# Kernel tuning notes

Measured on AMD Instinct MI355X. Metric: run time of the kernel, lower is better.

## Reference

```python
import jax, jax.numpy as jnp
import numpy as np

D_MODEL, D_K, D_FF, N = 1024, 128, 4096, 8192

def _linear_params(key, fan_in, fan_out):
    # mimic torch nn.Linear default init (uniform +/- 1/sqrt(fan_in))
    k1, k2 = jax.random.split(key)
    bound = 1.0 / np.sqrt(fan_in)
    W = jax.random.uniform(k1, (fan_out, fan_in), jnp.float32, -bound, bound)
    b = jax.random.uniform(k2, (fan_out,), jnp.float32, -bound, bound)
    return W, b

def setup_inputs() -> dict:
    key = jax.random.key(0)
    ks = jax.random.split(key, 7)
    x = jax.random.normal(ks[0], (N, D_MODEL), jnp.float32)
    Wq, bq = _linear_params(ks[1], D_MODEL, D_K)
    Wk, bk = _linear_params(ks[2], D_MODEL, D_K)
    Wv, bv = _linear_params(ks[3], D_MODEL, D_K)
    Wp, bp = _linear_params(ks[4], D_K, D_MODEL)
    W1, b1 = _linear_params(ks[5], D_MODEL, D_FF)
    W2, b2 = _linear_params(ks[6], D_FF, D_MODEL)
    return {"x": x, "Wq": Wq, "bq": bq, "Wk": Wk, "bk": bk, "Wv": Wv, "bv": bv,
            "Wp": Wp, "bp": bp, "W1": W1, "b1": b1, "W2": W2, "b2": b2}

def reference(x, Wq, bq, Wk, bk, Wv, bv, Wp, bp, W1, b1, W2, b2):
    # projections (torch Linear: x @ W.T + b)
    Q = x @ Wq.T + bq            # [n, d_k]
    K = x @ Wk.T + bk            # [n, d_k]
    V = x @ Wv.T + bv            # [n, d_k]
    # linear attention, original evaluation order: (Q @ K^T) @ V
    attn = Q @ K.T               # [n, n]
    context = attn @ V           # [n, d_k]
    out = context @ Wp.T + bp    # [n, d_model]
    x = x + out                  # residual 1
    h = jax.nn.relu(x @ W1.T + b1)  # [n, d_ff]
    return x + (h @ W2.T + b2)   # residual 2
```

## Files before the change

kernel.cpp:

```cpp
#include <hip/hip_runtime.h>


#define MROWS 8192
#define DMODEL 1024
#define DK 128
#define DFF 4096

typedef __attribute__((ext_vector_type(8))) __bf16 bf16x8;
typedef __attribute__((ext_vector_type(4))) float f32x4;

#define BAR()     __builtin_amdgcn_s_barrier()
#define WAITV(n)  asm volatile("s_waitcnt vmcnt(" #n ")" ::: "memory")
#define LGKMC(n)  asm volatile("s_waitcnt lgkmcnt(" #n ")" ::: "memory")
#define SCHED0()  __builtin_amdgcn_sched_barrier(0)
#define GLOAD(src, dst) __builtin_amdgcn_global_load_lds( \
    (const __attribute__((address_space(1))) void*)(src), \
    (__attribute__((address_space(3))) void*)(dst), 16, 0, 0)

#define LDSO(p) ((unsigned)(unsigned long long) \
    (__attribute__((address_space(3))) const char*)(const char*)(p))

__device__ __forceinline__ bf16x8 ldsr(unsigned off) {
    bf16x8 r;
    asm volatile("ds_read_b128 %0, %1" : "=v"(r) : "v"(off));
    return r;
}

__device__ __forceinline__ void cast_one(const float* s, __bf16* d, int i) {
    const float4 a = reinterpret_cast<const float4*>(s)[2 * i];
    const float4 b = reinterpret_cast<const float4*>(s)[2 * i + 1];
    bf16x8 o;
    o[0] = (__bf16)a.x; o[1] = (__bf16)a.y; o[2] = (__bf16)a.z; o[3] = (__bf16)a.w;
    o[4] = (__bf16)b.x; o[5] = (__bf16)b.y; o[6] = (__bf16)b.z; o[7] = (__bf16)b.w;
    reinterpret_cast<bf16x8*>(d)[i] = o;
}

__global__ __launch_bounds__(256) void cast6(
    const float* __restrict__ s0, __bf16* __restrict__ d0,
    const float* __restrict__ s1, __bf16* __restrict__ d1,
    const float* __restrict__ s2, __bf16* __restrict__ d2,
    const float* __restrict__ s3, __bf16* __restrict__ d3,
    const float* __restrict__ s4, __bf16* __restrict__ d4,
    const float* __restrict__ s5, __bf16* __restrict__ d5)
{
    const int b = blockIdx.x, t = threadIdx.x;
    if      (b <  64)  cast_one(s0, d0, b * 256 + t);
    else if (b < 128)  cast_one(s1, d1, (b - 64) * 256 + t);
    else if (b < 192)  cast_one(s2, d2, (b - 128) * 256 + t);
    else if (b < 256)  cast_one(s3, d3, (b - 192) * 256 + t);
    else if (b < 2304) cast_one(s4, d4, (b - 256) * 256 + t);
    else               cast_one(s5, d5, (b - 2304) * 256 + t);
}

__global__ void pack_bias3(const float* __restrict__ a, const float* __restrict__ b,
                           const float* __restrict__ c, float* __restrict__ o)
{
    const int t = threadIdx.x;
    o[t] = a[t]; o[128 + t] = b[t]; o[256 + t] = c[t];
}

__global__ __launch_bounds__(256) void ffn2_reduce2(
    float* __restrict__ y, const __bf16* __restrict__ x2b,
    const __bf16* __restrict__ P0, const __bf16* __restrict__ P1,
    const float* __restrict__ b2, int n8)
{
    for (int i = blockIdx.x * blockDim.x + threadIdx.x; i < n8;
         i += gridDim.x * blockDim.x) {
        const int col0 = (i << 3) & (DMODEL - 1);
        const float4 ba = *reinterpret_cast<const float4*>(&b2[col0]);
        const float4 bb = *reinterpret_cast<const float4*>(&b2[col0 + 4]);
        const bf16x8 xx = reinterpret_cast<const bf16x8*>(x2b)[i];
        const bf16x8 p0 = reinterpret_cast<const bf16x8*>(P0)[i];
        const bf16x8 p1 = reinterpret_cast<const bf16x8*>(P1)[i];
        float4 o0, o1;
        o0.x = (float)xx[0] + (float)p0[0] + (float)p1[0] + ba.x;
        o0.y = (float)xx[1] + (float)p0[1] + (float)p1[1] + ba.y;
        o0.z = (float)xx[2] + (float)p0[2] + (float)p1[2] + ba.z;
        o0.w = (float)xx[3] + (float)p0[3] + (float)p1[3] + ba.w;
        o1.x = (float)xx[4] + (float)p0[4] + (float)p1[4] + bb.x;
        o1.y = (float)xx[5] + (float)p0[5] + (float)p1[5] + bb.y;
        o1.z = (float)xx[6] + (float)p0[6] + (float)p1[6] + bb.z;
        o1.w = (float)xx[7] + (float)p0[7] + (float)p1[7] + bb.w;
        reinterpret_cast<float4*>(y)[2 * i]     = o0;
        reinterpret_cast<float4*>(y)[2 * i + 1] = o1;
    }
}

template<bool RELU, bool RESID, bool BIAS, bool OUTBF, bool DUAL, bool F32A>
__global__ __launch_bounds__(256) void gemm128(
    const void* __restrict__ Ap, int lda,
    const __bf16* __restrict__ W,
    const float* __restrict__ bias,
    const float* __restrict__ resid,
    void* __restrict__ Cout, __bf16* __restrict__ Cbf, int ldc, int K)
{
    constexpr int BK = 32;
    __shared__ __bf16 As[128 * BK];
    __shared__ __bf16 Bs[128 * BK];

    const int tid  = threadIdx.x;
    const int lane = tid & 63;
    const int w    = tid >> 6;
    const int wm   = w >> 1;
    const int wn   = w & 1;
    const int fr   = lane & 15;
    const int fq   = lane >> 4;

    const long row0 = (long)blockIdx.y * 128;
    const long col0 = (long)blockIdx.x * 128;

    const int sr = (w << 4) + (lane >> 2);
    const int sc = (lane & 3) << 3;

    const __bf16* gA0 = F32A ? nullptr : (const __bf16*)Ap + (row0 + sr) * (long)lda + sc;
    const __bf16* gA1 = F32A ? nullptr : (const __bf16*)Ap + (row0 + 64 + sr) * (long)lda + sc;
    const float*  gAf = F32A ? (const float*)Ap + (row0 + (tid >> 1)) * (long)lda
                               + ((tid & 1) << 4)
                             : nullptr;
    const __bf16* gW0 = W + (col0 + sr) * (long)K + sc;
    const __bf16* gW1 = W + (col0 + 64 + sr) * (long)K + sc;

    __bf16* lA0 = &As[(w << 4) * BK];
    __bf16* lA1 = &As[((w << 4) + 64) * BK];
    __bf16* lB0 = &Bs[(w << 4) * BK];
    __bf16* lB1 = &Bs[((w << 4) + 64) * BK];

    f32x4 acc[4][4] = {};

    for (int k0 = 0; k0 < K; k0 += BK) {
        if constexpr (F32A) {
            const float* s = gAf + k0;
            const float4 f0 = reinterpret_cast<const float4*>(s)[0];
            const float4 f1 = reinterpret_cast<const float4*>(s)[1];
            const float4 f2 = reinterpret_cast<const float4*>(s)[2];
            const float4 f3 = reinterpret_cast<const float4*>(s)[3];
            bf16x8 o0, o1;
            o0[0] = (__bf16)f0.x; o0[1] = (__bf16)f0.y; o0[2] = (__bf16)f0.z; o0[3] = (__bf16)f0.w;
            o0[4] = (__bf16)f1.x; o0[5] = (__bf16)f1.y; o0[6] = (__bf16)f1.z; o0[7] = (__bf16)f1.w;
            o1[0] = (__bf16)f2.x; o1[1] = (__bf16)f2.y; o1[2] = (__bf16)f2.z; o1[3] = (__bf16)f2.w;
            o1[4] = (__bf16)f3.x; o1[5] = (__bf16)f3.y; o1[6] = (__bf16)f3.z; o1[7] = (__bf16)f3.w;
            const int ar = tid >> 1, ac = (tid & 1) << 4;
            *reinterpret_cast<bf16x8*>(&As[ar * BK + ac])     = o0;
            *reinterpret_cast<bf16x8*>(&As[ar * BK + ac + 8]) = o1;
        } else {
            GLOAD(gA0 + k0, lA0);
            GLOAD(gA1 + k0, lA1);
        }
        GLOAD(gW0 + k0, lB0);
        GLOAD(gW1 + k0, lB1);
        __syncthreads();

        bf16x8 af[4], bfr[4];
        #pragma unroll
        for (int m = 0; m < 4; m++)
            af[m] = *reinterpret_cast<const bf16x8*>(
                &As[(wm * 64 + m * 16 + fr) * BK + fq * 8]);
        #pragma unroll
        for (int n = 0; n < 4; n++)
            bfr[n] = *reinterpret_cast<const bf16x8*>(
                &Bs[(wn * 64 + n * 16 + fr) * BK + fq * 8]);

        #pragma unroll
        for (int m = 0; m < 4; m++)
            #pragma unroll
            for (int n = 0; n < 4; n++)
                acc[m][n] = __builtin_amdgcn_mfma_f32_16x16x32_bf16(
                    af[m], bfr[n], acc[m][n], 0, 0, 0);
        __syncthreads();
    }

    float bc[4];
    #pragma unroll
    for (int n = 0; n < 4; n++)
        bc[n] = BIAS ? bias[col0 + wn * 64 + n * 16 + fr] : 0.0f;
    #pragma unroll
    for (int m = 0; m < 4; m++) {
        #pragma unroll
        for (int j = 0; j < 4; j++) {
            const long r = row0 + wm * 64 + m * 16 + fq * 4 + j;
            #pragma unroll
            for (int n = 0; n < 4; n++) {
                const long c = col0 + wn * 64 + n * 16 + fr;
                float v = acc[m][n][j] + bc[n];
                if constexpr (RESID) v += resid[r * ldc + c];
                if constexpr (RELU)  v = fmaxf(v, 0.0f);
                if constexpr (OUTBF) ((__bf16*)Cout)[r * ldc + c] = (__bf16)v;
                else                 ((float*)Cout)[r * ldc + c] = v;
                if constexpr (DUAL)  Cbf[r * ldc + c] = (__bf16)v;
            }
        }
    }
}

#define RD_B()                                             \
    _Pragma("unroll")                                      \
    for (int n = 0; n < 4; n++) {                          \
        bb[n][0] = ldsr(pB + rb0 + n * 2048);              \
        bb[n][1] = ldsr(pB + rb1 + n * 2048);              \
    }
#define RD_A(m0_, cnt_)                                    \
    _Pragma("unroll")                                      \
    for (int m = m0_; m < m0_ + cnt_; m++) {               \
        a[m][0] = ldsr(pA + rb0 + m * 2048);               \
        a[m][1] = ldsr(pA + rb1 + m * 2048);               \
    }
#define MFMA2(m0_)                                                            \
    _Pragma("unroll")                                                         \
    for (int m = m0_; m < m0_ + 2; m++)                                       \
        _Pragma("unroll")                                                     \
        for (int n = 0; n < 4; n++) {                                         \
            acc[m][n] = __builtin_amdgcn_mfma_f32_16x16x32_bf16(              \
                a[m][0], bb[n][0], acc[m][n], 0, 0, 0);                       \
            acc[m][n] = __builtin_amdgcn_mfma_f32_16x16x32_bf16(              \
                a[m][1], bb[n][1], acc[m][n], 0, 0, 0);                       \
        }

template<bool RELU, bool BIAS>
__global__ __launch_bounds__(256, 2) void gemm256x128(
    const __bf16* __restrict__ A, int lda,
    const __bf16* __restrict__ W, int ldw,
    const float* __restrict__ bias,
    __bf16* __restrict__ Cout, long sstride, int ldc,
    int klen, int nb, int nbx)
{
    __shared__ char lds[49152];

    const int bid = blockIdx.x;
    const int sid = bid / nb;
    const int ib  = bid % nb;
    const int chunk = nb >> 3;
    const int swz   = (ib & 7) * chunk + (ib >> 3);
    const int bx    = swz % nbx;
    const int by    = swz / nbx;

    const long row0 = (long)by * 256;
    const long col0 = (long)bx * 128;

    const __bf16* Ash = A + (long)sid * klen;
    const __bf16* Wsh = W + (long)sid * klen;

    const int tid  = threadIdx.x;
    const int lane = tid & 63;
    const int w    = tid >> 6;
    const int wm   = w >> 1;
    const int wn   = w & 1;
    const int fr   = lane & 15;
    const int fq   = lane >> 4;

    const int scole = ((lane & 7) ^ (lane >> 3)) << 3;
    const __bf16* gA = Ash + (row0 + w * 8 + (lane >> 3)) * (long)lda + scole;
    const __bf16* gB = Wsh + (col0 + w * 8 + (lane >> 3)) * (long)ldw + scole;

    char* ldsc = &lds[0];
    const unsigned lbase = LDSO(ldsc);
    const int nt = klen >> 6;

    auto stage = [&](int t) {
        const __bf16* ap = gA + (long)t * 64;
        const __bf16* bp = gB + (long)t * 64;
        #pragma unroll
        for (int r = 0; r < 8; r++)
            GLOAD(ap + (long)(32 * r) * lda, ldsc + r * 4096 + (w << 10));
        #pragma unroll
        for (int r = 0; r < 4; r++)
            GLOAD(bp + (long)(32 * r) * ldw, ldsc + 32768 + r * 4096 + (w << 10));
    };

    const unsigned rb0 = fr * 128 + ((fq * 16) ^ ((fr & 7) << 4));
    const unsigned rb1 = fr * 128 + ((64 + fq * 16) ^ ((fr & 7) << 4));
    const unsigned pA = lbase + (wm << 14);
    const unsigned pB = lbase + 32768 + (wn << 13);

    f32x4 acc[8][4] = {};
    bf16x8 a[8][2], bb[4][2];

    for (int t = 0; t < nt; ++t) {
        stage(t);
        WAITV(0);
        BAR();

        RD_B();
        RD_A(0, 8);

        LGKMC(12); SCHED0();
        __builtin_amdgcn_s_setprio(1); MFMA2(0); __builtin_amdgcn_s_setprio(0);
        LGKMC(8); SCHED0();
        __builtin_amdgcn_s_setprio(1); MFMA2(2); __builtin_amdgcn_s_setprio(0);
        LGKMC(4); SCHED0();
        __builtin_amdgcn_s_setprio(1); MFMA2(4); __builtin_amdgcn_s_setprio(0);
        LGKMC(0); SCHED0();
        __builtin_amdgcn_s_setprio(1); MFMA2(6); __builtin_amdgcn_s_setprio(0);

        BAR();
    }

    __bf16* Cb = Cout + (long)sid * sstride;
    float bc[4];
    #pragma unroll
    for (int n = 0; n < 4; n++)
        bc[n] = BIAS ? bias[col0 + wn * 64 + n * 16 + fr] : 0.0f;

    __bf16* sw = reinterpret_cast<__bf16*>(ldsc) + (w << 12);
    const long crow0 = row0 + wm * 128;
    const long ccol0 = col0 + wn * 64;
    #pragma unroll
    for (int half = 0; half < 2; half++) {
        #pragma unroll
        for (int m = 0; m < 4; m++)
            #pragma unroll
            for (int j = 0; j < 4; j++) {
                const int row = m * 16 + fq * 4 + j;
                #pragma unroll
                for (int n = 0; n < 4; n++) {
                    float v = acc[half * 4 + m][n][j] + bc[n];
                    if constexpr (RELU) v = fmaxf(v, 0.0f);
                    sw[row * 64 + n * 16 + fr] = (__bf16)v;
                }
            }
        #pragma unroll
        for (int i = 0; i < 8; i++) {
            const bf16x8 vv = *reinterpret_cast<const bf16x8*>(sw + i * 512 + lane * 8);
            const int r  = half * 64 + i * 8 + (lane >> 3);
            const int cg = (lane & 7) << 3;
            *reinterpret_cast<bf16x8*>(&Cb[(crow0 + r) * (long)ldc + ccol0 + cg]) = vv;
        }
        __builtin_amdgcn_s_waitcnt(0);
    }
}

__global__ __launch_bounds__(256) void ktv_partial(
    const __bf16* __restrict__ Kp, const __bf16* __restrict__ Vp,
    int ld, float* __restrict__ part)
{
    __shared__ float ks[32][DK];
    __shared__ float vs[32][DK];
    const int tid = threadIdx.x;
    const int ti  = tid >> 4;
    const int tj  = tid & 15;
    float acc[8][8] = {};
    const long base = (long)blockIdx.x * 128;

    for (int n0 = 0; n0 < 128; n0 += 32) {
        for (int t = tid; t < 512; t += 256) {
            const int r  = t >> 4;
            const int cc = (t & 15) << 3;
            const bf16x8 k8 = *reinterpret_cast<const bf16x8*>(
                &Kp[(base + n0 + r) * (long)ld + cc]);
            const bf16x8 v8 = *reinterpret_cast<const bf16x8*>(
                &Vp[(base + n0 + r) * (long)ld + cc]);
            #pragma unroll
            for (int u = 0; u < 8; u++) {
                ks[r][cc + u] = (float)k8[u];
                vs[r][cc + u] = (float)v8[u];
            }
        }
        __syncthreads();
        for (int n = 0; n < 32; n++) {
            float kk[8], vv[8];
            #pragma unroll
            for (int i = 0; i < 8; i++) kk[i] = ks[n][(ti << 3) + i];
            #pragma unroll
            for (int j = 0; j < 8; j++) vv[j] = vs[n][(tj << 3) + j];
            #pragma unroll
            for (int i = 0; i < 8; i++)
                #pragma unroll
                for (int j = 0; j < 8; j++)
                    acc[i][j] = fmaf(kk[i], vv[j], acc[i][j]);
        }
        __syncthreads();
    }

    float* dst = &part[(long)blockIdx.x * (DK * DK)];
    #pragma unroll
    for (int i = 0; i < 8; i++) {
        const int ig = (ti << 3) + i;
        *reinterpret_cast<float4*>(&dst[ig * DK + (tj << 3)]) =
            make_float4(acc[i][0], acc[i][1], acc[i][2], acc[i][3]);
        *reinterpret_cast<float4*>(&dst[ig * DK + (tj << 3) + 4]) =
            make_float4(acc[i][4], acc[i][5], acc[i][6], acc[i][7]);
    }
}

__global__ __launch_bounds__(256) void ktv_reduce(
    const float* __restrict__ part, __bf16* __restrict__ ktvR)
{
    const int t = blockIdx.x * 256 + threadIdx.x;
    float s = 0.0f;
    for (int b = 0; b < 64; b++) s += part[(long)b * (DK * DK) + t];
    ktvR[t] = (__bf16)s;
}

extern "C" void kernel_launch(void* const* d_in, const int* in_sizes, int n_in,
                              void* d_out, int out_size, void* d_ws, size_t ws_size,
                              hipStream_t stream) {
    const float* x  = (const float*)d_in[0];
    const float* Wq = (const float*)d_in[1];
    const float* bq = (const float*)d_in[2];
    const float* Wk = (const float*)d_in[3];
    const float* bk = (const float*)d_in[4];
    const float* Wv = (const float*)d_in[5];
    const float* bv = (const float*)d_in[6];
    const float* Wp = (const float*)d_in[7];
    const float* bp = (const float*)d_in[8];
    const float* W1 = (const float*)d_in[9];
    const float* b1 = (const float*)d_in[10];
    const float* W2 = (const float*)d_in[11];
    const float* b2 = (const float*)d_in[12];
    float* out = (float*)d_out;

    char* ws = (char*)d_ws;
    const size_t MB = 1ull << 20;
    __bf16* P0b   = (__bf16*)(ws);
    __bf16* P1b   = P0b + (long)MROWS * DMODEL;
    __bf16* x2b   = (__bf16*)(ws +  34 * MB);
    __bf16* Hb    = (__bf16*)(ws +  51 * MB);
    __bf16* QKVb  = (__bf16*)(ws + 119 * MB);
    __bf16* W1b   = (__bf16*)(ws + 126 * MB);
    __bf16* W2b   = (__bf16*)(ws + 135 * MB);
    __bf16* Wqkvb = (__bf16*)(ws + 144 * MB);
    __bf16* Wpb   = (__bf16*)(ws + 145 * MB);
    float*  Part  = (float*) (ws + 146 * MB);
    __bf16* KtvRb = (__bf16*)(ws + 151 * MB);
    __bf16* MtB   = (__bf16*)(ws + 152 * MB);
    float*  bqkvf = (float*) (ws + 155 * MB);

    const dim3 blk(256);

    cast6<<<4352, blk, 0, stream>>>(
        Wq, Wqkvb, Wk, Wqkvb + DK * DMODEL, Wv, Wqkvb + 2 * DK * DMODEL,
        Wp, Wpb, W1, W1b, W2, W2b);
    pack_bias3<<<1, 128, 0, stream>>>(bq, bk, bv, bqkvf);

    gemm128<false,false,true,true,false,true><<<dim3(3, 64), blk, 0, stream>>>(
        x, DMODEL, Wqkvb, bqkvf, nullptr, QKVb, nullptr, 3 * DK, DMODEL);

    ktv_partial<<<64, blk, 0, stream>>>(QKVb + DK, QKVb + 2 * DK, 3 * DK, Part);
    ktv_reduce <<<64, blk, 0, stream>>>(Part, KtvRb);

    gemm128<false,false,false,true,false,false><<<dim3(1, 8), blk, 0, stream>>>(
        Wpb, DK, KtvRb, nullptr, nullptr, MtB, nullptr, DK, DK);

    gemm128<false,true,true,true,false,false><<<dim3(8, 64), blk, 0, stream>>>(
        QKVb, 3 * DK, MtB, bp, x, x2b, nullptr, DMODEL, DK);

    gemm256x128<true,true><<<1024, blk, 0, stream>>>(
        x2b, DMODEL, W1b, DMODEL, b1, Hb, 0, DFF, DMODEL, 1024, DFF / 128);

    gemm256x128<false,false><<<512, blk, 0, stream>>>(
        Hb, DFF, W2b, DFF, nullptr, P0b,
        (long)MROWS * DMODEL, DMODEL, DFF / 2, 256, DMODEL / 128);

    ffn2_reduce2<<<2048, blk, 0, stream>>>(out, x2b, P0b, P1b, b2,
                                           MROWS * DMODEL / 8);
}
```

Baseline: 223.8 us.

## Double-buffer FFN GEMM LDS with K=32 stages and prefetch next tile

The FFN GEMM kernel switches from a single-buffered K=64 tile loop to a double-buffered K=32 loop. The next stage's global-to-LDS loads are issued right after the barrier, so they overlap the current stage's MFMAs, and the trailing per-iteration barrier is removed. The staging and swizzle layout is changed to match the 32-wide rows. The cost is twice as many iterations and barriers, with half as much MFMA work per barrier; LDS use stays within the 48KB buffer.

New measurement: 241.5 us. 1.08x slower.

```diff
diff --git a/kernel.cpp b/kernel.cpp
--- a/kernel.cpp
+++ b/kernel.cpp
@@ -192,31 +192,16 @@
     }
 }
 
-#define RD_B()                                             \
-    _Pragma("unroll")                                      \
-    for (int n = 0; n < 4; n++) {                          \
-        bb[n][0] = ldsr(pB + rb0 + n * 2048);              \
-        bb[n][1] = ldsr(pB + rb1 + n * 2048);              \
-    }
-#define RD_A(m0_, cnt_)                                    \
-    _Pragma("unroll")                                      \
-    for (int m = m0_; m < m0_ + cnt_; m++) {               \
-        a[m][0] = ldsr(pA + rb0 + m * 2048);               \
-        a[m][1] = ldsr(pA + rb1 + m * 2048);               \
-    }
-#define MFMA2(m0_)                                                            \
+#define MFMA2S(m0_)                                                           \
     _Pragma("unroll")                                                         \
     for (int m = m0_; m < m0_ + 2; m++)                                       \
         _Pragma("unroll")                                                     \
-        for (int n = 0; n < 4; n++) {                                         \
+        for (int n = 0; n < 4; n++)                                           \
             acc[m][n] = __builtin_amdgcn_mfma_f32_16x16x32_bf16(              \
-                a[m][0], bb[n][0], acc[m][n], 0, 0, 0);                       \
-            acc[m][n] = __builtin_amdgcn_mfma_f32_16x16x32_bf16(              \
-                a[m][1], bb[n][1], acc[m][n], 0, 0, 0);                       \
-        }
+                a[m], bb[n], acc[m][n], 0, 0, 0);
 
 template<bool RELU, bool BIAS>
-__global__ __launch_bounds__(256, 2) void gemm256x128(
+__global__ __launch_bounds__(256, 2) void gemm_ffn(
     const __bf16* __restrict__ A, int lda,
     const __bf16* __restrict__ W, int ldw,
     const float* __restrict__ bias,
@@ -247,52 +232,62 @@
     const int fr   = lane & 15;
     const int fq   = lane >> 4;
 
-    const int scole = ((lane & 7) ^ (lane >> 3)) << 3;
-    const __bf16* gA = Ash + (row0 + w * 8 + (lane >> 3)) * (long)lda + scole;
-    const __bf16* gB = Wsh + (col0 + w * 8 + (lane >> 3)) * (long)ldw + scole;
+    const int srow = ((lane >> 3) << 1) | ((lane >> 2) & 1);
+    const int scol = (((lane & 3) ^ ((lane >> 3) & 3)) << 3);
+    const __bf16* gA = Ash + (row0 + srow) * (long)lda + scol;
+    const __bf16* gB = Wsh + (col0 + srow) * (long)ldw + scol;
 
     char* ldsc = &lds[0];
     const unsigned lbase = LDSO(ldsc);
-    const int nt = klen >> 6;
-
-    auto stage = [&](int t) {
-        const __bf16* ap = gA + (long)t * 64;
-        const __bf16* bp = gB + (long)t * 64;
-        #pragma unroll
-        for (int r = 0; r < 8; r++)
-            GLOAD(ap + (long)(32 * r) * lda, ldsc + r * 4096 + (w << 10));
-        #pragma unroll
-        for (int r = 0; r < 4; r++)
-            GLOAD(bp + (long)(32 * r) * ldw, ldsc + 32768 + r * 4096 + (w << 10));
+    const int nt = klen >> 5;
+
+    auto stage = [&](int t, unsigned boff) {
+        const __bf16* ap = gA + (long)t * 32;
+        const __bf16* bp = gB + (long)t * 32;
+        #pragma unroll
+        for (int r = 0; r < 4; r++) {
+            const int c = r * 4 + w;
+            GLOAD(ap + (long)(c * 16) * lda, ldsc + boff + c * 1024);
+        }
+        #pragma unroll
+        for (int r = 0; r < 2; r++) {
+            const int c = r * 4 + w;
+            GLOAD(bp + (long)(c * 16) * ldw, ldsc + boff + 16384 + c * 1024);
+        }
     };
 
-    const unsigned rb0 = fr * 128 + ((fq * 16) ^ ((fr & 7) << 4));
-    const unsigned rb1 = fr * 128 + ((64 + fq * 16) ^ ((fr & 7) << 4));
-    const unsigned pA = lbase + (wm << 14);
-    const unsigned pB = lbase + 32768 + (wn << 13);
+    const unsigned rbA = ((fr >> 1) << 7) + ((fr & 1) << 6)
+                       + ((fq ^ ((fr >> 1) & 3)) << 4);
+    const unsigned pAo = (unsigned)(wm << 13);
+    const unsigned pBo = 16384u + (unsigned)(wn << 12);
 
     f32x4 acc[8][4] = {};
-    bf16x8 a[8][2], bb[4][2];
-
+    bf16x8 a[8], bb[4];
+
+    stage(0, 0);
     for (int t = 0; t < nt; ++t) {
-        stage(t);
+        const unsigned boff = (t & 1) ? 24576u : 0u;
         WAITV(0);
         BAR();
-
-        RD_B();
-        RD_A(0, 8);
-
-        LGKMC(12); SCHED0();
-        __builtin_amdgcn_s_setprio(1); MFMA2(0); __builtin_amdgcn_s_setprio(0);
-        LGKMC(8); SCHED0();
-        __builtin_amdgcn_s_setprio(1); MFMA2(2); __builtin_amdgcn_s_setprio(0);
+        if (t + 1 < nt) stage(t + 1, boff ^ 24576u);
+
+        const unsigned pA = lbase + boff + pAo;
+        const unsigned pB = lbase + boff + pBo;
+        #pragma unroll
+        for (int n = 0; n < 4; n++) bb[n] = ldsr(pB + rbA + n * 1024);
+        #pragma unroll
+        for (int m = 0; m < 8; m++) a[m] = ldsr(pA + rbA + m * 1024);
+
+        LGKMC(6); SCHED0();
+        __builtin_amdgcn_s_setprio(1); MFMA2S(0); __builtin_amdgcn_s_setprio(0);
         LGKMC(4); SCHED0();
-        __builtin_amdgcn_s_setprio(1); MFMA2(4); __builtin_amdgcn_s_setprio(0);
+        __builtin_amdgcn_s_setprio(1); MFMA2S(2); __builtin_amdgcn_s_setprio(0);
+        LGKMC(2); SCHED0();
+        __builtin_amdgcn_s_setprio(1); MFMA2S(4); __builtin_amdgcn_s_setprio(0);
         LGKMC(0); SCHED0();
-        __builtin_amdgcn_s_setprio(1); MFMA2(6); __builtin_amdgcn_s_setprio(0);
-
-        BAR();
-    }
+        __builtin_amdgcn_s_setprio(1); MFMA2S(6); __builtin_amdgcn_s_setprio(0);
+    }
+    BAR();
 
     __bf16* Cb = Cout + (long)sid * sstride;
     float bc[4];
@@ -443,10 +438,10 @@
     gemm128<false,true,true,true,false,false><<<dim3(8, 64), blk, 0, stream>>>(
         QKVb, 3 * DK, MtB, bp, x, x2b, nullptr, DMODEL, DK);
 
-    gemm256x128<true,true><<<1024, blk, 0, stream>>>(
+    gemm_ffn<true,true><<<1024, blk, 0, stream>>>(
         x2b, DMODEL, W1b, DMODEL, b1, Hb, 0, DFF, DMODEL, 1024, DFF / 128);
 
-    gemm256x128<false,false><<<512, blk, 0, stream>>>(
+    gemm_ffn<false,false><<<512, blk, 0, stream>>>(
         Hb, DFF, W2b, DFF, nullptr, P0b,
         (long)MROWS * DMODEL, DMODEL, DFF / 2, 256, DMODEL / 128);
 
```
